# Optimization experiments

Hardware: AMD Instinct MI355X
Metric: run time of the kernel (lower is better)

Reference implementation:

```python
import jax, jax.numpy as jnp
import numpy as np

EPS = 1e-5

def _ln(x, g, b):
    m = jnp.mean(x, axis=-1, keepdims=True)
    v = jnp.mean(jnp.square(x - m), axis=-1, keepdims=True)
    return (x - m) * jax.lax.rsqrt(v + EPS) * g + b

def setup_inputs() -> dict:
    key = jax.random.key(0)
    ks = jax.random.split(key, 20)
    B, F = 262144, 768
    sizes = [F, 512, 256, 128, 1]  # LN(d_in) -> Linear(d_in, d_out) per block
    inp = {"input": jax.random.normal(ks[0], (B, F), dtype=jnp.float32)}
    for i in range(4):
        din, dout = sizes[i], sizes[i + 1]
        inp[f"g{i}"] = jnp.ones((din,), dtype=jnp.float32)
        inp[f"b{i}"] = jnp.zeros((din,), dtype=jnp.float32)
        bound = 1.0 / np.sqrt(din)
        inp[f"W{i}"] = jax.random.uniform(ks[1 + 2 * i], (dout, din), dtype=jnp.float32, minval=-bound, maxval=bound)
        inp[f"c{i}"] = jax.random.uniform(ks[2 + 2 * i], (dout,), dtype=jnp.float32, minval=-bound, maxval=bound)
    return inp

def reference(input, g0, b0, W0, c0, g1, b1, W1, c1, g2, b2, W2, c2, g3, b3, W3, c3):
    x = input
    params = [(g0, b0, W0, c0), (g1, b1, W1, c1), (g2, b2, W2, c2), (g3, b3, W3, c3)]
    for i, (g, b, W, c) in enumerate(params):
        x = _ln(x, g, b)
        x = x @ W.T + c
        if i != 3:
            x = jax.nn.elu(x)
    return jnp.squeeze(x, axis=-1)  # [B]
```

## Files before the change

### kernel.cpp

```cpp
#include <hip/hip_runtime.h>
#include <hip/hip_fp16.h>
#include <math.h>

typedef _Float16 half_t;
typedef half_t half4_t __attribute__((ext_vector_type(4)));
typedef half_t half8_t __attribute__((ext_vector_type(8)));
typedef float f32x4 __attribute__((ext_vector_type(4)));

#define LN_EPS 1e-5f

__global__ void pack_weights(const float* __restrict__ W0, const float* __restrict__ g0,
                             const float* __restrict__ W1, const float* __restrict__ g1,
                             const float* __restrict__ W2, const float* __restrict__ g2,
                             half_t* __restrict__ ws) {
    int sid = blockIdx.x * 256 + threadIdx.x;
    const float* W; const float* g; int K, T, off;
    if (sid < 49152)      { W = W0; g = g0; K = 768; T = 24; off = 0; }
    else if (sid < 65536) { W = W1; g = g1; K = 512; T = 16; off = 49152; sid -= 49152; }
    else if (sid < 69632) { W = W2; g = g2; K = 256; T = 8;  off = 65536; sid -= 65536; }
    else return;
    const int l   = sid & 63;
    const int t   = (sid >> 6) % T;
    const int cbg = (sid >> 6) / T;
    const int n   = (l & 15) + 16 * cbg;
    const int k0  = 32 * t + 8 * (l >> 4);
    const float* src = W + (size_t)n * K + k0;
    const float* gs  = g + k0;
    half8_t v;
    #pragma unroll
    for (int jq = 0; jq < 8; jq++) v[jq] = (half_t)(src[jq] * gs[jq]);
    *(half8_t*)(ws + (size_t)(off + sid) * 8) = v;
}

__global__ void fold_bias(const float* __restrict__ W0, const float* __restrict__ g0,
                          const float* __restrict__ b0, const float* __restrict__ c0,
                          const float* __restrict__ W1, const float* __restrict__ g1,
                          const float* __restrict__ b1, const float* __restrict__ c1,
                          const float* __restrict__ W2, const float* __restrict__ g2,
                          const float* __restrict__ b2, const float* __restrict__ c2,
                          const float* __restrict__ W3, const float* __restrict__ g3,
                          const float* __restrict__ b3, const float* __restrict__ c3,
                          float* __restrict__ f) {
    const int gw   = (blockIdx.x * 256 + threadIdx.x) >> 6;
    const int lane = threadIdx.x & 63;
    if (gw == 896) {
        float s = 0.f, cb_ = 0.f;
        for (int k = lane; k < 128; k += 64) {
            const float wg = W3[k] * g3[k];
            f[1792 + k] = wg;
            s += wg; cb_ += W3[k] * b3[k];
        }
        #pragma unroll
        for (int m = 1; m < 64; m <<= 1) { s += __shfl_xor(s, m); cb_ += __shfl_xor(cb_, m); }
        if (lane == 0) { f[1920] = s; f[1921] = cb_ + c3[0]; }
        return;
    }
    const float *W, *g, *b, *cc; int K, n; float *sf, *cf;
    if (gw < 512)      { W = W0; g = g0; b = b0; cc = c0; K = 768; n = gw;       sf = f;        cf = f + 512; }
    else if (gw < 768) { W = W1; g = g1; b = b1; cc = c1; K = 512; n = gw - 512; sf = f + 1024; cf = f + 1280; }
    else if (gw < 896) { W = W2; g = g2; b = b2; cc = c2; K = 256; n = gw - 768; sf = f + 1536; cf = f + 1664; }
    else return;
    const float* Wr = W + (size_t)n * K;
    float s = 0.f, cb_ = 0.f;
    for (int k = lane; k < K; k += 64) { const float wg = Wr[k] * g[k]; s += wg; cb_ += Wr[k] * b[k]; }
    #pragma unroll
    for (int m = 1; m < 64; m <<= 1) { s += __shfl_xor(s, m); cb_ += __shfl_xor(cb_, m); }
    if (lane == 0) { sf[n] = s; cf[n] = cb_ + cc[n]; }
}

__global__ __launch_bounds__(512, 4)
void fused_mlp(const float* __restrict__ x_in,
               const half_t* __restrict__ W0p, const half_t* __restrict__ W1p,
               const half_t* __restrict__ W2p, const float* __restrict__ f,
               float* __restrict__ out)
{
    __shared__ half_t frag[32768];
    __shared__ float row_m[64], row_rs[64];
    __shared__ float w3s[128];

    const int tid  = threadIdx.x;
    const int lane = tid & 63;
    const int wv   = tid >> 6;
    const int grp  = lane >> 4;
    const int cl   = lane & 15;
    const int row  = tid >> 3;
    const int jj   = tid & 7;
    const int rbw  = row >> 4;
    const long r0  = (long)blockIdx.x * 64;
    const float* xrow = x_in + (r0 + row) * 768;

    const float* s0f = f;        const float* c0f = f + 512;
    const float* s1f = f + 1024; const float* c1f = f + 1280;
    const float* s2f = f + 1536; const float* c2f = f + 1664;

    if (tid < 128) w3s[tid] = f[1792 + tid];

    float s = 0.f, ss = 0.f;
    f32x4 vb[4];

    auto stage_load = [&](int c) {
        const float* xp = xrow + 128 * c + 4 * jj;
        #pragma unroll
        for (int i = 0; i < 4; i++)
            vb[i] = __builtin_nontemporal_load((const f32x4*)(xp + 32 * i));
    };
    auto stage_write = [&](int c) {
        half_t* fb = frag + 8192 * (c & 1);
        const int hg = jj >> 1, jo = 4 * (jj & 1);
        #pragma unroll
        for (int i = 0; i < 4; i++) {
            const f32x4 v = vb[i];
            s  += v[0] + v[1] + v[2] + v[3];
            ss += v[0]*v[0] + v[1]*v[1] + v[2]*v[2] + v[3]*v[3];
            half4_t hv;
            hv[0] = (half_t)v[0]; hv[1] = (half_t)v[1];
            hv[2] = (half_t)v[2]; hv[3] = (half_t)v[3];
            *(half4_t*)(&fb[((i * 4 + rbw) * 64 + ((row & 15) + 16 * hg)) * 8 + jo]) = hv;
        }
    };

    f32x4 acc0[4][4];
    #pragma unroll
    for (int rb = 0; rb < 4; rb++)
        #pragma unroll
        for (int cb = 0; cb < 4; cb++) acc0[rb][cb] = 0.f;

    auto gemm0 = [&](int c) {
        const half_t* fb = frag + 8192 * (c & 1);
        const half_t* wp = W0p + (size_t)(4 * wv * 24 + 4 * c) * 512 + lane * 8;
        half8_t bA[4], bB[4];
        #pragma unroll
        for (int cb = 0; cb < 4; cb++) bA[cb] = *(const half8_t*)(wp + cb * 12288);
        #pragma unroll
        for (int tt = 0; tt < 4; tt++) {
            half8_t* cur = (tt & 1) ? bB : bA;
            half8_t* nxt = (tt & 1) ? bA : bB;
            if (tt < 3) {
                #pragma unroll
                for (int cb = 0; cb < 4; cb++)
                    nxt[cb] = *(const half8_t*)(wp + (tt + 1) * 512 + cb * 12288);
            }
            half8_t af[4];
            #pragma unroll
            for (int rb = 0; rb < 4; rb++)
                af[rb] = *(const half8_t*)(&fb[((tt * 4 + rb) * 64 + lane) * 8]);
            #pragma unroll
            for (int cb = 0; cb < 4; cb++)
                #pragma unroll
                for (int rb = 0; rb < 4; rb++)
                    acc0[rb][cb] = __builtin_amdgcn_mfma_f32_16x16x32_f16(af[rb], cur[cb], acc0[rb][cb], 0, 0, 0);
        }
    };

    stage_load(0); stage_write(0);
    __syncthreads();
    #pragma unroll 1
    for (int c = 0; c < 6; c++) {
        if (c < 5) stage_load(c + 1);
        gemm0(c);
        if (c < 5) stage_write(c + 1);
        if (c == 4) {
            s  += __shfl_xor(s, 1);  s  += __shfl_xor(s, 2);  s  += __shfl_xor(s, 4);
            ss += __shfl_xor(ss, 1); ss += __shfl_xor(ss, 2); ss += __shfl_xor(ss, 4);
            if (jj == 0) {
                const float mm = s * (1.f / 768.f);
                row_m[row]  = mm;
                row_rs[row] = 1.f / sqrtf(ss * (1.f / 768.f) - mm * mm + LN_EPS);
            }
        }
        __syncthreads();
    }

    {
        float sv[4], cv[4];
        #pragma unroll
        for (int cb = 0; cb < 4; cb++) {
            const int c = cl + 16 * (4 * wv + cb);
            sv[cb] = s0f[c]; cv[cb] = c0f[c];
        }
        #pragma unroll
        for (int rb = 0; rb < 4; rb++)
            #pragma unroll
            for (int v = 0; v < 4; v++) {
                const int r = 16 * rb + 4 * grp + v;
                const float rm = row_m[r], rr = row_rs[r];
                #pragma unroll
                for (int cb = 0; cb < 4; cb++) {
                    float y = rr * (acc0[rb][cb][v] - rm * sv[cb]) + cv[cb];
                    acc0[rb][cb][v] = y > 0.f ? y : (__expf(y) - 1.f);
                }
            }
        #pragma unroll
        for (int cb = 0; cb < 4; cb++) {
            const int c = cl + 16 * (4 * wv + cb);
            const int t = c >> 5, j = c & 7, sc = 16 * ((c >> 3) & 3);
            #pragma unroll
            for (int rb = 0; rb < 4; rb++)
                #pragma unroll
                for (int v = 0; v < 4; v++)
                    frag[((t * 4 + rb) * 64 + (4 * grp + v + sc)) * 8 + j] = (half_t)acc0[rb][cb][v];
        }
    }
    __syncthreads();

    {
        const int r15 = row & 15, rb = row >> 4;
        float s_ = 0.f, q_ = 0.f;
        #pragma unroll
        for (int i = 0; i < 8; i++) {
            const int ch = jj + 8 * i;
            const int t = ch >> 2, cg = ch & 3;
            const half8_t h = *(const half8_t*)(frag + (size_t)((t * 4 + rb) * 64 + r15 + 16 * cg) * 8);
            #pragma unroll
            for (int e = 0; e < 8; e++) { const float fv = (float)h[e]; s_ += fv; q_ += fv * fv; }
        }
        s_ += __shfl_xor(s_, 1); s_ += __shfl_xor(s_, 2); s_ += __shfl_xor(s_, 4);
        q_ += __shfl_xor(q_, 1); q_ += __shfl_xor(q_, 2); q_ += __shfl_xor(q_, 4);
        if (jj == 0) {
            const float mm = s_ * (1.f / 512.f);
            row_m[row]  = mm;
            row_rs[row] = 1.f / sqrtf(q_ * (1.f / 512.f) - mm * mm + LN_EPS);
        }
    }

    f32x4 acc1[4][2];
    #pragma unroll
    for (int rb = 0; rb < 4; rb++) { acc1[rb][0] = 0.f; acc1[rb][1] = 0.f; }
    {
        const half_t* wp = W1p + (size_t)(2 * wv * 16) * 512 + lane * 8;
        half8_t bA[2], bB[2];
        bA[0] = *(const half8_t*)(wp);
        bA[1] = *(const half8_t*)(wp + 8192);
        #pragma unroll
        for (int t = 0; t < 16; t++) {
            half8_t* cur = (t & 1) ? bB : bA;
            half8_t* nxt = (t & 1) ? bA : bB;
            if (t < 15) {
                nxt[0] = *(const half8_t*)(wp + (t + 1) * 512);
                nxt[1] = *(const half8_t*)(wp + (t + 1) * 512 + 8192);
            }
            half8_t af[4];
            #pragma unroll
            for (int rb = 0; rb < 4; rb++)
                af[rb] = *(const half8_t*)(&frag[((t * 4 + rb) * 64 + lane) * 8]);
            #pragma unroll
            for (int cb = 0; cb < 2; cb++)
                #pragma unroll
                for (int rb = 0; rb < 4; rb++)
                    acc1[rb][cb] = __builtin_amdgcn_mfma_f32_16x16x32_f16(af[rb], cur[cb], acc1[rb][cb], 0, 0, 0);
        }
    }
    __syncthreads();

    {
        float sv[2], cv[2];
        #pragma unroll
        for (int cb = 0; cb < 2; cb++) {
            const int c = cl + 16 * (2 * wv + cb);
            sv[cb] = s1f[c]; cv[cb] = c1f[c];
        }
        #pragma unroll
        for (int rb = 0; rb < 4; rb++)
            #pragma unroll
            for (int v = 0; v < 4; v++) {
                const int r = 16 * rb + 4 * grp + v;
                const float rm = row_m[r], rr = row_rs[r];
                #pragma unroll
                for (int cb = 0; cb < 2; cb++) {
                    float y = rr * (acc1[rb][cb][v] - rm * sv[cb]) + cv[cb];
                    acc1[rb][cb][v] = y > 0.f ? y : (__expf(y) - 1.f);
                }
            }
        #pragma unroll
        for (int cb = 0; cb < 2; cb++) {
            const int c = cl + 16 * (2 * wv + cb);
            const int t = c >> 5, j = c & 7, sc = 16 * ((c >> 3) & 3);
            #pragma unroll
            for (int rb = 0; rb < 4; rb++)
                #pragma unroll
                for (int v = 0; v < 4; v++)
                    frag[((t * 4 + rb) * 64 + (4 * grp + v + sc)) * 8 + j] = (half_t)acc1[rb][cb][v];
        }
    }
    __syncthreads();

    {
        const int r15 = row & 15, rb = row >> 4;
        float s_ = 0.f, q_ = 0.f;
        #pragma unroll
        for (int i = 0; i < 4; i++) {
            const int ch = jj + 8 * i;
            const int t = ch >> 2, cg = ch & 3;
            const half8_t h = *(const half8_t*)(frag + (size_t)((t * 4 + rb) * 64 + r15 + 16 * cg) * 8);
            #pragma unroll
            for (int e = 0; e < 8; e++) { const float fv = (float)h[e]; s_ += fv; q_ += fv * fv; }
        }
        s_ += __shfl_xor(s_, 1); s_ += __shfl_xor(s_, 2); s_ += __shfl_xor(s_, 4);
        q_ += __shfl_xor(q_, 1); q_ += __shfl_xor(q_, 2); q_ += __shfl_xor(q_, 4);
        if (jj == 0) {
            const float mm = s_ * (1.f / 256.f);
            row_m[row]  = mm;
            row_rs[row] = 1.f / sqrtf(q_ * (1.f / 256.f) - mm * mm + LN_EPS);
        }
    }

    f32x4 acc2[4];
    #pragma unroll
    for (int rb = 0; rb < 4; rb++) acc2[rb] = 0.f;
    {
        const half_t* wp = W2p + (size_t)(wv * 8) * 512 + lane * 8;
        half8_t bA = *(const half8_t*)(wp);
        #pragma unroll
        for (int t = 0; t < 8; t++) {
            const half8_t cur = bA;
            if (t < 7) bA = *(const half8_t*)(wp + (t + 1) * 512);
            half8_t af[4];
            #pragma unroll
            for (int rb = 0; rb < 4; rb++)
                af[rb] = *(const half8_t*)(&frag[((t * 4 + rb) * 64 + lane) * 8]);
            #pragma unroll
            for (int rb = 0; rb < 4; rb++)
                acc2[rb] = __builtin_amdgcn_mfma_f32_16x16x32_f16(af[rb], cur, acc2[rb], 0, 0, 0);
        }
    }
    __syncthreads();

    {
        const int c2i = cl + 16 * wv;
        const float sv = s2f[c2i], cv = c2f[c2i];
        #pragma unroll
        for (int rb = 0; rb < 4; rb++)
            #pragma unroll
            for (int v = 0; v < 4; v++) {
                const int r = 16 * rb + 4 * grp + v;
                const float rm = row_m[r], rr = row_rs[r];
                float y = rr * (acc2[rb][v] - rm * sv) + cv;
                y = y > 0.f ? y : (__expf(y) - 1.f);
                frag[r * 136 + c2i] = (half_t)y;
            }
    }
    __syncthreads();

    {
        float s_ = 0.f, q_ = 0.f, d_ = 0.f;
        #pragma unroll
        for (int u = 0; u < 2; u++) {
            const int cb = jj * 16 + 8 * u;
            const half8_t h = *(const half8_t*)(frag + row * 136 + cb);
            #pragma unroll
            for (int e = 0; e < 8; e++) {
                const float fv = (float)h[e];
                s_ += fv; q_ += fv * fv; d_ += fv * w3s[cb + e];
            }
        }
        s_ += __shfl_xor(s_, 1); s_ += __shfl_xor(s_, 2); s_ += __shfl_xor(s_, 4);
        q_ += __shfl_xor(q_, 1); q_ += __shfl_xor(q_, 2); q_ += __shfl_xor(q_, 4);
        d_ += __shfl_xor(d_, 1); d_ += __shfl_xor(d_, 2); d_ += __shfl_xor(d_, 4);
        if (jj == 0) {
            const float mm = s_ * (1.f / 128.f);
            const float rs = 1.f / sqrtf(q_ * (1.f / 128.f) - mm * mm + LN_EPS);
            out[r0 + row] = rs * (d_ - mm * f[1920]) + f[1921];
        }
    }
}

extern "C" void kernel_launch(void* const* d_in, const int* in_sizes, int n_in,
                              void* d_out, int out_size, void* d_ws, size_t ws_size,
                              hipStream_t stream) {
    const float* x  = (const float*)d_in[0];
    const float* g0 = (const float*)d_in[1];
    const float* b0 = (const float*)d_in[2];
    const float* W0 = (const float*)d_in[3];
    const float* c0 = (const float*)d_in[4];
    const float* g1 = (const float*)d_in[5];
    const float* b1 = (const float*)d_in[6];
    const float* W1 = (const float*)d_in[7];
    const float* c1 = (const float*)d_in[8];
    const float* g2 = (const float*)d_in[9];
    const float* b2 = (const float*)d_in[10];
    const float* W2 = (const float*)d_in[11];
    const float* c2 = (const float*)d_in[12];
    const float* g3 = (const float*)d_in[13];
    const float* b3 = (const float*)d_in[14];
    const float* W3 = (const float*)d_in[15];
    const float* c3 = (const float*)d_in[16];

    half_t* ws = (half_t*)d_ws;
    float*  f  = (float*)(ws + 557056);

    pack_weights<<<272, 256, 0, stream>>>(W0, g0, W1, g1, W2, g2, ws);
    fold_bias<<<225, 256, 0, stream>>>(W0, g0, b0, c0, W1, g1, b1, c1,
                                       W2, g2, b2, c2, W3, g3, b3, c3, f);

    const int nrows = in_sizes[0] / 768;
    fused_mlp<<<nrows / 64, 512, 0, stream>>>(
        x, ws, ws + 393216, ws + 524288, f, (float*)d_out);
}
```

Baseline: 548.0 us.

## Load layer-0 activations directly into MFMA registers, skipping LDS staging

The first GEMM no longer stages x through shared memory with double buffering and per-chunk barriers. Each wave now loads its A fragments straight from global memory into registers, converts them to fp16, and feeds the MFMAs. Waves are split 2 (row halves) by 4 (column quarters) instead of splitting only by columns. Each wave computes LayerNorm statistics for its slice of K, and the partial sums are combined through a small LDS array. This removes LDS traffic and barriers, but each wave reloads the same x rows, so global and L2 reads of the input go up about fourfold, nontemporal hints are dropped, and the fully unrolled loop raises register pressure.

```diff
diff --git a/kernel.cpp b/kernel.cpp
--- a/kernel.cpp
+++ b/kernel.cpp
@@ -75,6 +75,7 @@
                float* __restrict__ out)
 {
     __shared__ half_t frag[32768];
+    __shared__ float ps[4][64], pq[4][64];
     __shared__ float row_m[64], row_rs[64];
     __shared__ float w3s[128];
 
@@ -85,9 +86,10 @@
     const int cl   = lane & 15;
     const int row  = tid >> 3;
     const int jj   = tid & 7;
-    const int rbw  = row >> 4;
     const long r0  = (long)blockIdx.x * 64;
-    const float* xrow = x_in + (r0 + row) * 768;
+
+    const int h = wv >> 2;
+    const int q = wv & 3;
 
     const float* s0f = f;        const float* c0f = f + 512;
     const float* s1f = f + 1024; const float* c1f = f + 1280;
@@ -95,111 +97,92 @@
 
     if (tid < 128) w3s[tid] = f[1792 + tid];
 
-    float s = 0.f, ss = 0.f;
-    f32x4 vb[4];
-
-    auto stage_load = [&](int c) {
-        const float* xp = xrow + 128 * c + 4 * jj;
-        #pragma unroll
-        for (int i = 0; i < 4; i++)
-            vb[i] = __builtin_nontemporal_load((const f32x4*)(xp + 32 * i));
-    };
-    auto stage_write = [&](int c) {
-        half_t* fb = frag + 8192 * (c & 1);
-        const int hg = jj >> 1, jo = 4 * (jj & 1);
-        #pragma unroll
-        for (int i = 0; i < 4; i++) {
-            const f32x4 v = vb[i];
-            s  += v[0] + v[1] + v[2] + v[3];
-            ss += v[0]*v[0] + v[1]*v[1] + v[2]*v[2] + v[3]*v[3];
-            half4_t hv;
-            hv[0] = (half_t)v[0]; hv[1] = (half_t)v[1];
-            hv[2] = (half_t)v[2]; hv[3] = (half_t)v[3];
-            *(half4_t*)(&fb[((i * 4 + rbw) * 64 + ((row & 15) + 16 * hg)) * 8 + jo]) = hv;
-        }
-    };
-
-    f32x4 acc0[4][4];
-    #pragma unroll
-    for (int rb = 0; rb < 4; rb++)
-        #pragma unroll
-        for (int cb = 0; cb < 4; cb++) acc0[rb][cb] = 0.f;
-
-    auto gemm0 = [&](int c) {
-        const half_t* fb = frag + 8192 * (c & 1);
-        const half_t* wp = W0p + (size_t)(4 * wv * 24 + 4 * c) * 512 + lane * 8;
-        half8_t bA[4], bB[4];
-        #pragma unroll
-        for (int cb = 0; cb < 4; cb++) bA[cb] = *(const half8_t*)(wp + cb * 12288);
-        #pragma unroll
-        for (int tt = 0; tt < 4; tt++) {
-            half8_t* cur = (tt & 1) ? bB : bA;
-            half8_t* nxt = (tt & 1) ? bA : bB;
-            if (tt < 3) {
-                #pragma unroll
-                for (int cb = 0; cb < 4; cb++)
-                    nxt[cb] = *(const half8_t*)(wp + (tt + 1) * 512 + cb * 12288);
-            }
-            half8_t af[4];
-            #pragma unroll
-            for (int rb = 0; rb < 4; rb++)
-                af[rb] = *(const half8_t*)(&fb[((tt * 4 + rb) * 64 + lane) * 8]);
-            #pragma unroll
-            for (int cb = 0; cb < 4; cb++)
-                #pragma unroll
-                for (int rb = 0; rb < 4; rb++)
-                    acc0[rb][cb] = __builtin_amdgcn_mfma_f32_16x16x32_f16(af[rb], cur[cb], acc0[rb][cb], 0, 0, 0);
-        }
-    };
-
-    stage_load(0); stage_write(0);
-    __syncthreads();
-    #pragma unroll 1
-    for (int c = 0; c < 6; c++) {
-        if (c < 5) stage_load(c + 1);
-        gemm0(c);
-        if (c < 5) stage_write(c + 1);
-        if (c == 4) {
-            s  += __shfl_xor(s, 1);  s  += __shfl_xor(s, 2);  s  += __shfl_xor(s, 4);
-            ss += __shfl_xor(ss, 1); ss += __shfl_xor(ss, 2); ss += __shfl_xor(ss, 4);
-            if (jj == 0) {
-                const float mm = s * (1.f / 768.f);
-                row_m[row]  = mm;
-                row_rs[row] = 1.f / sqrtf(ss * (1.f / 768.f) - mm * mm + LN_EPS);
-            }
-        }
-        __syncthreads();
-    }
-
-    {
-        float sv[4], cv[4];
-        #pragma unroll
-        for (int cb = 0; cb < 4; cb++) {
-            const int c = cl + 16 * (4 * wv + cb);
+    const float* xr0 = x_in + (r0 + 32 * h + cl) * 768 + 8 * grp;
+    const float* xr1 = xr0 + 16 * 768;
+    const half_t* wq = W0p + (size_t)(8 * q) * 12288 + lane * 8;
+
+    f32x4 acc0[2][8];
+    #pragma unroll
+    for (int rb = 0; rb < 2; rb++)
+        #pragma unroll
+        for (int cb = 0; cb < 8; cb++) acc0[rb][cb] = 0.f;
+
+    float s0 = 0.f, q0 = 0.f, s1 = 0.f, q1 = 0.f;
+
+    #pragma unroll
+    for (int tg = 0; tg < 4; tg++) {
+        const bool mine = (tg == q);
+        #pragma unroll
+        for (int tt = 0; tt < 6; tt++) {
+            const int t = 6 * tg + tt;
+            const f32x4 a00 = *(const f32x4*)(xr0 + 32 * t);
+            const f32x4 a01 = *(const f32x4*)(xr0 + 32 * t + 4);
+            const f32x4 a10 = *(const f32x4*)(xr1 + 32 * t);
+            const f32x4 a11 = *(const f32x4*)(xr1 + 32 * t + 4);
+            if (mine) {
+                #pragma unroll
+                for (int e = 0; e < 4; e++) {
+                    s0 += a00[e] + a01[e]; q0 += a00[e]*a00[e] + a01[e]*a01[e];
+                    s1 += a10[e] + a11[e]; q1 += a10[e]*a10[e] + a11[e]*a11[e];
+                }
+            }
+            half8_t h0, h1;
+            #pragma unroll
+            for (int e = 0; e < 4; e++) {
+                h0[e] = (half_t)a00[e]; h0[4 + e] = (half_t)a01[e];
+                h1[e] = (half_t)a10[e]; h1[4 + e] = (half_t)a11[e];
+            }
+            #pragma unroll
+            for (int cbp = 0; cbp < 4; cbp++) {
+                const half8_t b0 = *(const half8_t*)(wq + (size_t)(2 * cbp) * 12288 + t * 512);
+                const half8_t b1 = *(const half8_t*)(wq + (size_t)(2 * cbp + 1) * 12288 + t * 512);
+                acc0[0][2*cbp]   = __builtin_amdgcn_mfma_f32_16x16x32_f16(h0, b0, acc0[0][2*cbp],   0, 0, 0);
+                acc0[1][2*cbp]   = __builtin_amdgcn_mfma_f32_16x16x32_f16(h1, b0, acc0[1][2*cbp],   0, 0, 0);
+                acc0[0][2*cbp+1] = __builtin_amdgcn_mfma_f32_16x16x32_f16(h0, b1, acc0[0][2*cbp+1], 0, 0, 0);
+                acc0[1][2*cbp+1] = __builtin_amdgcn_mfma_f32_16x16x32_f16(h1, b1, acc0[1][2*cbp+1], 0, 0, 0);
+            }
+        }
+    }
+
+    s0 += __shfl_xor(s0, 16); s0 += __shfl_xor(s0, 32);
+    q0 += __shfl_xor(q0, 16); q0 += __shfl_xor(q0, 32);
+    s1 += __shfl_xor(s1, 16); s1 += __shfl_xor(s1, 32);
+    q1 += __shfl_xor(q1, 16); q1 += __shfl_xor(q1, 32);
+    if (grp == 0) {
+        ps[q][32 * h + cl]      = s0;  pq[q][32 * h + cl]      = q0;
+        ps[q][32 * h + 16 + cl] = s1;  pq[q][32 * h + 16 + cl] = q1;
+    }
+    __syncthreads();
+    if (tid < 64) {
+        const float a_ = ps[0][tid] + ps[1][tid] + ps[2][tid] + ps[3][tid];
+        const float b_ = pq[0][tid] + pq[1][tid] + pq[2][tid] + pq[3][tid];
+        const float mm = a_ * (1.f / 768.f);
+        row_m[tid]  = mm;
+        row_rs[tid] = 1.f / sqrtf(b_ * (1.f / 768.f) - mm * mm + LN_EPS);
+    }
+    __syncthreads();
+
+    {
+        float sv[8], cv[8];
+        #pragma unroll
+        for (int cb = 0; cb < 8; cb++) {
+            const int c = cl + 16 * (8 * q + cb);
             sv[cb] = s0f[c]; cv[cb] = c0f[c];
         }
         #pragma unroll
-        for (int rb = 0; rb < 4; rb++)
+        for (int rb = 0; rb < 2; rb++)
             #pragma unroll
             for (int v = 0; v < 4; v++) {
-                const int r = 16 * rb + 4 * grp + v;
+                const int r = 32 * h + 16 * rb + 4 * grp + v;
                 const float rm = row_m[r], rr = row_rs[r];
                 #pragma unroll
-                for (int cb = 0; cb < 4; cb++) {
+                for (int cb = 0; cb < 8; cb++) {
                     float y = rr * (acc0[rb][cb][v] - rm * sv[cb]) + cv[cb];
-                    acc0[rb][cb][v] = y > 0.f ? y : (__expf(y) - 1.f);
+                    y = y > 0.f ? y : (__expf(y) - 1.f);
+                    const int c = cl + 16 * (8 * q + cb);
+                    frag[(((c >> 5) * 4 + (2 * h + rb)) * 64 + (4 * grp + v + 16 * ((c >> 3) & 3))) * 8 + (c & 7)] = (half_t)y;
                 }
             }
-        #pragma unroll
-        for (int cb = 0; cb < 4; cb++) {
-            const int c = cl + 16 * (4 * wv + cb);
-            const int t = c >> 5, j = c & 7, sc = 16 * ((c >> 3) & 3);
-            #pragma unroll
-            for (int rb = 0; rb < 4; rb++)
-                #pragma unroll
-                for (int v = 0; v < 4; v++)
-                    frag[((t * 4 + rb) * 64 + (4 * grp + v + sc)) * 8 + j] = (half_t)acc0[rb][cb][v];
-        }
     }
     __syncthreads();
 
@@ -210,9 +193,9 @@
         for (int i = 0; i < 8; i++) {
             const int ch = jj + 8 * i;
             const int t = ch >> 2, cg = ch & 3;
-            const half8_t h = *(const half8_t*)(frag + (size_t)((t * 4 + rb) * 64 + r15 + 16 * cg) * 8);
-            #pragma unroll
-            for (int e = 0; e < 8; e++) { const float fv = (float)h[e]; s_ += fv; q_ += fv * fv; }
+            const half8_t hh = *(const half8_t*)(frag + (size_t)((t * 4 + rb) * 64 + r15 + 16 * cg) * 8);
+            #pragma unroll
+            for (int e = 0; e < 8; e++) { const float fv = (float)hh[e]; s_ += fv; q_ += fv * fv; }
         }
         s_ += __shfl_xor(s_, 1); s_ += __shfl_xor(s_, 2); s_ += __shfl_xor(s_, 4);
         q_ += __shfl_xor(q_, 1); q_ += __shfl_xor(q_, 2); q_ += __shfl_xor(q_, 4);
@@ -291,9 +274,9 @@
         for (int i = 0; i < 4; i++) {
             const int ch = jj + 8 * i;
             const int t = ch >> 2, cg = ch & 3;
-            const half8_t h = *(const half8_t*)(frag + (size_t)((t * 4 + rb) * 64 + r15 + 16 * cg) * 8);
-            #pragma unroll
-            for (int e = 0; e < 8; e++) { const float fv = (float)h[e]; s_ += fv; q_ += fv * fv; }
+            const half8_t hh = *(const half8_t*)(frag + (size_t)((t * 4 + rb) * 64 + r15 + 16 * cg) * 8);
+            #pragma unroll
+            for (int e = 0; e < 8; e++) { const float fv = (float)hh[e]; s_ += fv; q_ += fv * fv; }
         }
         s_ += __shfl_xor(s_, 1); s_ += __shfl_xor(s_, 2); s_ += __shfl_xor(s_, 4);
         q_ += __shfl_xor(q_, 1); q_ += __shfl_xor(q_, 2); q_ += __shfl_xor(q_, 4);
@@ -346,10 +329,10 @@
         #pragma unroll
         for (int u = 0; u < 2; u++) {
             const int cb = jj * 16 + 8 * u;
-            const half8_t h = *(const half8_t*)(frag + row * 136 + cb);
+            const half8_t hh = *(const half8_t*)(frag + row * 136 + cb);
             #pragma unroll
             for (int e = 0; e < 8; e++) {
-                const float fv = (float)h[e];
+                const float fv = (float)hh[e];
                 s_ += fv; q_ += fv * fv; d_ += fv * w3s[cb + e];
             }
         }
```

After: 704.5 us. 1.29x slower.

## Split waves over row halves and column quarters in all GEMM stages

Applied to the files above, without the earlier changes.

Work is redistributed across the 8 waves: each wave now owns 32 rows and a quarter of the output columns, instead of all 64 rows and an eighth of the columns. Each wave reads fewer A-fragments from LDS and streams more weight columns from global memory, trading LDS traffic for global/L2 weight loads. The first-layer weight prefetch double-buffering is dropped, and the ELU results are written straight to LDS rather than in a separate pass. Total weight traffic per block doubles, and exposed global load latency in gemm0 may grow.

```diff
diff --git a/kernel.cpp b/kernel.cpp
--- a/kernel.cpp
+++ b/kernel.cpp
@@ -89,6 +89,9 @@
     const long r0  = (long)blockIdx.x * 64;
     const float* xrow = x_in + (r0 + row) * 768;
 
+    const int h  = wv >> 2;
+    const int q  = wv & 3;
+
     const float* s0f = f;        const float* c0f = f + 512;
     const float* s1f = f + 1024; const float* c1f = f + 1280;
     const float* s2f = f + 1536; const float* c2f = f + 1664;
@@ -119,36 +122,27 @@
         }
     };
 
-    f32x4 acc0[4][4];
+    f32x4 acc0[2][8];
     #pragma unroll
-    for (int rb = 0; rb < 4; rb++)
-        #pragma unroll
-        for (int cb = 0; cb < 4; cb++) acc0[rb][cb] = 0.f;
+    for (int rb = 0; rb < 2; rb++)
+        #pragma unroll
+        for (int cb = 0; cb < 8; cb++) acc0[rb][cb] = 0.f;
 
     auto gemm0 = [&](int c) {
         const half_t* fb = frag + 8192 * (c & 1);
-        const half_t* wp = W0p + (size_t)(4 * wv * 24 + 4 * c) * 512 + lane * 8;
-        half8_t bA[4], bB[4];
-        #pragma unroll
-        for (int cb = 0; cb < 4; cb++) bA[cb] = *(const half8_t*)(wp + cb * 12288);
+        const half_t* wq = W0p + (size_t)(8 * q) * 12288 + (size_t)(4 * c) * 512 + lane * 8;
         #pragma unroll
         for (int tt = 0; tt < 4; tt++) {
-            half8_t* cur = (tt & 1) ? bB : bA;
-            half8_t* nxt = (tt & 1) ? bA : bB;
-            if (tt < 3) {
-                #pragma unroll
-                for (int cb = 0; cb < 4; cb++)
-                    nxt[cb] = *(const half8_t*)(wp + (tt + 1) * 512 + cb * 12288);
-            }
-            half8_t af[4];
-            #pragma unroll
-            for (int rb = 0; rb < 4; rb++)
-                af[rb] = *(const half8_t*)(&fb[((tt * 4 + rb) * 64 + lane) * 8]);
-            #pragma unroll
-            for (int cb = 0; cb < 4; cb++)
-                #pragma unroll
-                for (int rb = 0; rb < 4; rb++)
-                    acc0[rb][cb] = __builtin_amdgcn_mfma_f32_16x16x32_f16(af[rb], cur[cb], acc0[rb][cb], 0, 0, 0);
+            half8_t af[2];
+            #pragma unroll
+            for (int rb = 0; rb < 2; rb++)
+                af[rb] = *(const half8_t*)(&fb[((tt * 4 + 2 * h + rb) * 64 + lane) * 8]);
+            #pragma unroll
+            for (int cb = 0; cb < 8; cb++) {
+                const half8_t bf = *(const half8_t*)(wq + (size_t)cb * 12288 + tt * 512);
+                acc0[0][cb] = __builtin_amdgcn_mfma_f32_16x16x32_f16(af[0], bf, acc0[0][cb], 0, 0, 0);
+                acc0[1][cb] = __builtin_amdgcn_mfma_f32_16x16x32_f16(af[1], bf, acc0[1][cb], 0, 0, 0);
+            }
         }
     };
 
@@ -172,34 +166,26 @@
     }
 
     {
-        float sv[4], cv[4];
-        #pragma unroll
-        for (int cb = 0; cb < 4; cb++) {
-            const int c = cl + 16 * (4 * wv + cb);
+        float sv[8], cv[8];
+        #pragma unroll
+        for (int cb = 0; cb < 8; cb++) {
+            const int c = cl + 16 * (8 * q + cb);
             sv[cb] = s0f[c]; cv[cb] = c0f[c];
         }
         #pragma unroll
-        for (int rb = 0; rb < 4; rb++)
+        for (int rb = 0; rb < 2; rb++)
             #pragma unroll
             for (int v = 0; v < 4; v++) {
-                const int r = 16 * rb + 4 * grp + v;
+                const int r = 32 * h + 16 * rb + 4 * grp + v;
                 const float rm = row_m[r], rr = row_rs[r];
                 #pragma unroll
-                for (int cb = 0; cb < 4; cb++) {
+                for (int cb = 0; cb < 8; cb++) {
                     float y = rr * (acc0[rb][cb][v] - rm * sv[cb]) + cv[cb];
-                    acc0[rb][cb][v] = y > 0.f ? y : (__expf(y) - 1.f);
+                    y = y > 0.f ? y : (__expf(y) - 1.f);
+                    const int c = cl + 16 * (8 * q + cb);
+                    frag[(((c >> 5) * 4 + (2 * h + rb)) * 64 + (4 * grp + v + 16 * ((c >> 3) & 3))) * 8 + (c & 7)] = (half_t)y;
                 }
             }
-        #pragma unroll
-        for (int cb = 0; cb < 4; cb++) {
-            const int c = cl + 16 * (4 * wv + cb);
-            const int t = c >> 5, j = c & 7, sc = 16 * ((c >> 3) & 3);
-            #pragma unroll
-            for (int rb = 0; rb < 4; rb++)
-                #pragma unroll
-                for (int v = 0; v < 4; v++)
-                    frag[((t * 4 + rb) * 64 + (4 * grp + v + sc)) * 8 + j] = (half_t)acc0[rb][cb][v];
-        }
     }
     __syncthreads();
 
@@ -210,9 +196,9 @@
         for (int i = 0; i < 8; i++) {
             const int ch = jj + 8 * i;
             const int t = ch >> 2, cg = ch & 3;
-            const half8_t h = *(const half8_t*)(frag + (size_t)((t * 4 + rb) * 64 + r15 + 16 * cg) * 8);
-            #pragma unroll
-            for (int e = 0; e < 8; e++) { const float fv = (float)h[e]; s_ += fv; q_ += fv * fv; }
+            const half8_t hh = *(const half8_t*)(frag + (size_t)((t * 4 + rb) * 64 + r15 + 16 * cg) * 8);
+            #pragma unroll
+            for (int e = 0; e < 8; e++) { const float fv = (float)hh[e]; s_ += fv; q_ += fv * fv; }
         }
         s_ += __shfl_xor(s_, 1); s_ += __shfl_xor(s_, 2); s_ += __shfl_xor(s_, 4);
         q_ += __shfl_xor(q_, 1); q_ += __shfl_xor(q_, 2); q_ += __shfl_xor(q_, 4);
@@ -223,64 +209,59 @@
         }
     }
 
-    f32x4 acc1[4][2];
+    f32x4 acc1[2][4];
     #pragma unroll
-    for (int rb = 0; rb < 4; rb++) { acc1[rb][0] = 0.f; acc1[rb][1] = 0.f; }
-    {
-        const half_t* wp = W1p + (size_t)(2 * wv * 16) * 512 + lane * 8;
-        half8_t bA[2], bB[2];
-        bA[0] = *(const half8_t*)(wp);
-        bA[1] = *(const half8_t*)(wp + 8192);
+    for (int rb = 0; rb < 2; rb++)
+        #pragma unroll
+        for (int cb = 0; cb < 4; cb++) acc1[rb][cb] = 0.f;
+    {
+        const half_t* wp = W1p + (size_t)(4 * q) * 8192 + lane * 8;
+        half8_t bA[4], bB[4];
+        #pragma unroll
+        for (int cb = 0; cb < 4; cb++) bA[cb] = *(const half8_t*)(wp + (size_t)cb * 8192);
         #pragma unroll
         for (int t = 0; t < 16; t++) {
             half8_t* cur = (t & 1) ? bB : bA;
             half8_t* nxt = (t & 1) ? bA : bB;
             if (t < 15) {
-                nxt[0] = *(const half8_t*)(wp + (t + 1) * 512);
-                nxt[1] = *(const half8_t*)(wp + (t + 1) * 512 + 8192);
-            }
-            half8_t af[4];
-            #pragma unroll
-            for (int rb = 0; rb < 4; rb++)
-                af[rb] = *(const half8_t*)(&frag[((t * 4 + rb) * 64 + lane) * 8]);
-            #pragma unroll
-            for (int cb = 0; cb < 2; cb++)
                 #pragma unroll
-                for (int rb = 0; rb < 4; rb++)
-                    acc1[rb][cb] = __builtin_amdgcn_mfma_f32_16x16x32_f16(af[rb], cur[cb], acc1[rb][cb], 0, 0, 0);
-        }
-    }
-    __syncthreads();
-
-    {
-        float sv[2], cv[2];
-        #pragma unroll
-        for (int cb = 0; cb < 2; cb++) {
-            const int c = cl + 16 * (2 * wv + cb);
+                for (int cb = 0; cb < 4; cb++)
+                    nxt[cb] = *(const half8_t*)(wp + (size_t)cb * 8192 + (t + 1) * 512);
+            }
+            half8_t af[2];
+            #pragma unroll
+            for (int rb = 0; rb < 2; rb++)
+                af[rb] = *(const half8_t*)(&frag[((t * 4 + 2 * h + rb) * 64 + lane) * 8]);
+            #pragma unroll
+            for (int cb = 0; cb < 4; cb++) {
+                acc1[0][cb] = __builtin_amdgcn_mfma_f32_16x16x32_f16(af[0], cur[cb], acc1[0][cb], 0, 0, 0);
+                acc1[1][cb] = __builtin_amdgcn_mfma_f32_16x16x32_f16(af[1], cur[cb], acc1[1][cb], 0, 0, 0);
+            }
+        }
+    }
+    __syncthreads();
+
+    {
+        float sv[4], cv[4];
+        #pragma unroll
+        for (int cb = 0; cb < 4; cb++) {
+            const int c = cl + 16 * (4 * q + cb);
             sv[cb] = s1f[c]; cv[cb] = c1f[c];
         }
         #pragma unroll
-        for (int rb = 0; rb < 4; rb++)
+        for (int rb = 0; rb < 2; rb++)
             #pragma unroll
             for (int v = 0; v < 4; v++) {
-                const int r = 16 * rb + 4 * grp + v;
+                const int r = 32 * h + 16 * rb + 4 * grp + v;
                 const float rm = row_m[r], rr = row_rs[r];
                 #pragma unroll
-                for (int cb = 0; cb < 2; cb++) {
+                for (int cb = 0; cb < 4; cb++) {
                     float y = rr * (acc1[rb][cb][v] - rm * sv[cb]) + cv[cb];
-                    acc1[rb][cb][v] = y > 0.f ? y : (__expf(y) - 1.f);
+                    y = y > 0.f ? y : (__expf(y) - 1.f);
+                    const int c = cl + 16 * (4 * q + cb);
+                    frag[(((c >> 5) * 4 + (2 * h + rb)) * 64 + (4 * grp + v + 16 * ((c >> 3) & 3))) * 8 + (c & 7)] = (half_t)y;
                 }
             }
-        #pragma unroll
-        for (int cb = 0; cb < 2; cb++) {
-            const int c = cl + 16 * (2 * wv + cb);
-            const int t = c >> 5, j = c & 7, sc = 16 * ((c >> 3) & 3);
-            #pragma unroll
-            for (int rb = 0; rb < 4; rb++)
-                #pragma unroll
-                for (int v = 0; v < 4; v++)
-                    frag[((t * 4 + rb) * 64 + (4 * grp + v + sc)) * 8 + j] = (half_t)acc1[rb][cb][v];
-        }
     }
     __syncthreads();
 
@@ -291,9 +272,9 @@
         for (int i = 0; i < 4; i++) {
             const int ch = jj + 8 * i;
             const int t = ch >> 2, cg = ch & 3;
-            const half8_t h = *(const half8_t*)(frag + (size_t)((t * 4 + rb) * 64 + r15 + 16 * cg) * 8);
-            #pragma unroll
-            for (int e = 0; e < 8; e++) { const float fv = (float)h[e]; s_ += fv; q_ += fv * fv; }
+            const half8_t hh = *(const half8_t*)(frag + (size_t)((t * 4 + rb) * 64 + r15 + 16 * cg) * 8);
+            #pragma unroll
+            for (int e = 0; e < 8; e++) { const float fv = (float)hh[e]; s_ += fv; q_ += fv * fv; }
         }
         s_ += __shfl_xor(s_, 1); s_ += __shfl_xor(s_, 2); s_ += __shfl_xor(s_, 4);
         q_ += __shfl_xor(q_, 1); q_ += __shfl_xor(q_, 2); q_ += __shfl_xor(q_, 4);
@@ -304,40 +285,48 @@
         }
     }
 
-    f32x4 acc2[4];
-    #pragma unroll
-    for (int rb = 0; rb < 4; rb++) acc2[rb] = 0.f;
-    {
-        const half_t* wp = W2p + (size_t)(wv * 8) * 512 + lane * 8;
-        half8_t bA = *(const half8_t*)(wp);
+    f32x4 acc2[2][2];
+    acc2[0][0] = 0.f; acc2[0][1] = 0.f; acc2[1][0] = 0.f; acc2[1][1] = 0.f;
+    {
+        const half_t* wp = W2p + (size_t)(2 * q) * 4096 + lane * 8;
+        half8_t bA[2];
+        bA[0] = *(const half8_t*)(wp);
+        bA[1] = *(const half8_t*)(wp + 4096);
         #pragma unroll
         for (int t = 0; t < 8; t++) {
-            const half8_t cur = bA;
-            if (t < 7) bA = *(const half8_t*)(wp + (t + 1) * 512);
-            half8_t af[4];
-            #pragma unroll
-            for (int rb = 0; rb < 4; rb++)
-                af[rb] = *(const half8_t*)(&frag[((t * 4 + rb) * 64 + lane) * 8]);
-            #pragma unroll
-            for (int rb = 0; rb < 4; rb++)
-                acc2[rb] = __builtin_amdgcn_mfma_f32_16x16x32_f16(af[rb], cur, acc2[rb], 0, 0, 0);
-        }
-    }
-    __syncthreads();
-
-    {
-        const int c2i = cl + 16 * wv;
-        const float sv = s2f[c2i], cv = c2f[c2i];
-        #pragma unroll
-        for (int rb = 0; rb < 4; rb++)
-            #pragma unroll
-            for (int v = 0; v < 4; v++) {
-                const int r = 16 * rb + 4 * grp + v;
-                const float rm = row_m[r], rr = row_rs[r];
-                float y = rr * (acc2[rb][v] - rm * sv) + cv;
-                y = y > 0.f ? y : (__expf(y) - 1.f);
-                frag[r * 136 + c2i] = (half_t)y;
-            }
+            const half8_t c0_ = bA[0], c1_ = bA[1];
+            if (t < 7) {
+                bA[0] = *(const half8_t*)(wp + (t + 1) * 512);
+                bA[1] = *(const half8_t*)(wp + 4096 + (t + 1) * 512);
+            }
+            half8_t af[2];
+            #pragma unroll
+            for (int rb = 0; rb < 2; rb++)
+                af[rb] = *(const half8_t*)(&frag[((t * 4 + 2 * h + rb) * 64 + lane) * 8]);
+            acc2[0][0] = __builtin_amdgcn_mfma_f32_16x16x32_f16(af[0], c0_, acc2[0][0], 0, 0, 0);
+            acc2[1][0] = __builtin_amdgcn_mfma_f32_16x16x32_f16(af[1], c0_, acc2[1][0], 0, 0, 0);
+            acc2[0][1] = __builtin_amdgcn_mfma_f32_16x16x32_f16(af[0], c1_, acc2[0][1], 0, 0, 0);
+            acc2[1][1] = __builtin_amdgcn_mfma_f32_16x16x32_f16(af[1], c1_, acc2[1][1], 0, 0, 0);
+        }
+    }
+    __syncthreads();
+
+    {
+        #pragma unroll
+        for (int cb = 0; cb < 2; cb++) {
+            const int c2i = cl + 16 * (2 * q + cb);
+            const float sv = s2f[c2i], cv = c2f[c2i];
+            #pragma unroll
+            for (int rb = 0; rb < 2; rb++)
+                #pragma unroll
+                for (int v = 0; v < 4; v++) {
+                    const int r = 32 * h + 16 * rb + 4 * grp + v;
+                    const float rm = row_m[r], rr = row_rs[r];
+                    float y = rr * (acc2[rb][cb][v] - rm * sv) + cv;
+                    y = y > 0.f ? y : (__expf(y) - 1.f);
+                    frag[r * 136 + c2i] = (half_t)y;
+                }
+        }
     }
     __syncthreads();
 
@@ -346,10 +335,10 @@
         #pragma unroll
         for (int u = 0; u < 2; u++) {
             const int cb = jj * 16 + 8 * u;
-            const half8_t h = *(const half8_t*)(frag + row * 136 + cb);
+            const half8_t hh = *(const half8_t*)(frag + row * 136 + cb);
             #pragma unroll
             for (int e = 0; e < 8; e++) {
-                const float fv = (float)h[e];
+                const float fv = (float)hh[e];
                 s_ += fv; q_ += fv * fv; d_ += fv * w3s[cb + e];
             }
         }
```

Measured after the change: 807.2 us. +47.3%, slower.
